# Performance work log

Hardware: AMD Instinct MI355X
Metric: run time of the kernel (lower is better)

Reference implementation:

```python
import jax, jax.numpy as jnp
import numpy as np

EMA_OLD = 0.01  # original: m[z] = m[z]*0.01 + y*0.99
EMA_NEW = 0.99

def setup_inputs() -> dict:
    key = jax.random.key(0)
    k1, k2, k3, k4 = jax.random.split(key, 4)
    B, n, C, L = 4096, 1024, 64, 64
    y = jax.random.normal(k1, (B, C, L), dtype=jnp.float32)   # encoder latents
    m = jax.random.normal(k2, (n, C, L), dtype=jnp.float32)   # codebook means
    sd = jax.random.uniform(k3, (n, C, L), dtype=jnp.float32) # codebook variances (init ones in orig)
    p = jax.random.uniform(k4, (n,), dtype=jnp.float32)       # cluster counts
    return {"y": y, "m": m, "sd": sd, "p": p}

def reference(y, m, sd, p):
    B, C, L = y.shape
    n = m.shape[0]
    # pairwise squared distances via ||y||^2 - 2 y.m + ||m||^2 (GEMM form)
    yf = y.reshape(B, C * L)
    mf = m.reshape(n, C * L)
    d2 = ((yf * yf).sum(-1, keepdims=True)
          - 2.0 * (yf @ mf.T)
          + (mf * mf).sum(-1)[None, :])            # [B, n]
    z = jnp.argmin(d2, axis=1)                      # [B] assignments
    new_m = m.at[z].set(m[z] * EMA_OLD + y * EMA_NEW)
    # original updates sd using the ALREADY-updated m gathered at z
    mg = new_m[z]
    new_sd = sd.at[z].set((mg - y) ** 2 * EMA_OLD + sd[z] * EMA_NEW)
    return jnp.concatenate([new_m, new_sd], axis=0)  # [2n, C, L]
```

## Files before the change

### kernel.cpp

```cpp
#include <hip/hip_runtime.h>

#define B_ROWS 4096
#define N_CLUST 1024
#define KDIM 4096
#define NKT 32
#define NSTEP 16

#define EMA_OLD 0.01f
#define EMA_NEW 0.99f
#define MARGIN 2.0f
#define PSCALE 16.0f

typedef unsigned short ushortT;
typedef _Float16 half8 __attribute__((ext_vector_type(8)));
typedef float f32x16 __attribute__((ext_vector_type(16)));

#define WS_WINNER_OFF 0
#define WS_Z_OFF      4096
#define WS_YY_OFF     20480
#define WS_MM_OFF     36864
#define WS_P_OFF      65536
#define WS_YHI_OFF    (WS_P_OFF + 33554432)
#define WS_MHI_OFF    (WS_YHI_OFF + 33554432)
#define WS_END        (WS_MHI_OFF + 8388608)

__global__ __launch_bounds__(256) void convert_sumsq(
    const float* __restrict__ ysrc, const float* __restrict__ msrc,
    ushortT* __restrict__ yhi, ushortT* __restrict__ mhi,
    float* __restrict__ yy, float* __restrict__ mm) {
    const int blk = blockIdx.x;
    const float* src;
    ushortT* hi;
    float* out;
    int row;
    if (blk < B_ROWS) {
        src = ysrc; hi = yhi; out = yy + blk; row = blk;
    } else {
        row = blk - B_ROWS;
        src = msrc; hi = mhi; out = mm + row;
    }
    const int r = row & 63, rb = row >> 6;
    const int t = threadIdx.x;
    float s = 0.f;
#pragma unroll
    for (int h = 0; h < 2; ++h) {
        int ci = h * 256 + t;
        int kt = ci >> 4, p = ci & 15;
        int c = p ^ (r & 15);
        const float* sp = src + ((size_t)row << 12) + kt * 128 + c * 8;
        float4 v0 = *(const float4*)sp;
        float4 v1 = *(const float4*)(sp + 4);
        float vv[8] = {v0.x, v0.y, v0.z, v0.w, v1.x, v1.y, v1.z, v1.w};
        half8 hv;
#pragma unroll
        for (int i = 0; i < 8; ++i) {
            hv[i] = (_Float16)vv[i];
            s += vv[i] * vv[i];
        }
        size_t off = (((size_t)rb * NKT + kt) * 64 + r) * 128 + p * 8;
        *(half8*)(hi + off) = hv;
    }
    for (int off = 32; off > 0; off >>= 1) s += __shfl_down(s, off, 64);
    __shared__ float red[4];
    if ((t & 63) == 0) red[t >> 6] = s;
    __syncthreads();
    if (t == 0) out[0] = red[0] + red[1] + red[2] + red[3];
}

__device__ __forceinline__ void gload_lds16(const void* g, void* l) {
    __builtin_amdgcn_global_load_lds(
        (const __attribute__((address_space(1))) unsigned int*)g,
        (__attribute__((address_space(3))) unsigned int*)l, 16, 0, 0);
}

__device__ __forceinline__ half8 ldfrag_pair(const ushortT* s, int r, int c) {
    int q = r >> 1;
    int sl = ((((r & 1) << 3) | c) ^ (q & 15));
    return *(const half8*)(s + q * 128 + sl * 8);
}

__global__ __launch_bounds__(256, 4) void screen_gemm(
    const ushortT* __restrict__ Ah, const ushortT* __restrict__ Bh,
    short* __restrict__ pws) {
    __shared__ __align__(16) ushortT sA[128 * 64];
    __shared__ __align__(16) ushortT sB[128 * 64];

    const int t = threadIdx.x, w = t >> 6, l = t & 63;
    const int by = blockIdx.x & 7;
    const int kh = (blockIdx.x >> 3) & 3;
    const int bx = blockIdx.x >> 5;
    const int row0 = bx * 128, col0 = by * 128;
    const int wr = (w >> 1) * 64, wc = (w & 1) * 64;
    const int m0 = l & 31, hsel = l >> 5;

    int laneoff[4];
#pragma unroll
    for (int j = 0; j < 4; ++j) {
        int g = w * 4 + j;
        int q = g * 4 + (l >> 4);
        int u = (l & 15) ^ (q & 15);
        int rr = 2 * q + (u >> 3);
        int R = rr & 63;
        int hi3 = (R >> 3) & 1;
        laneoff[j] = R * 256 + ((((hi3 << 3) | ((u & 7) ^ (R & 7)))) << 4);
    }

    f32x16 acc[2][2];
#pragma unroll
    for (int i = 0; i < 2; ++i)
#pragma unroll
        for (int j = 0; j < 2; ++j)
#pragma unroll
            for (int r = 0; r < 16; ++r) acc[i][j][r] = 0.f;

    const int ra0 = wr + m0, ra1 = wr + 32 + m0;
    const int rb0 = wc + m0, rb1 = wc + 32 + m0;

#pragma unroll 2
    for (int i = 0; i < NSTEP; ++i) {
        const int kt_ = kh * (NKT / 4) + (i >> 1);
        const int ks_ = i & 1;
        __syncthreads();
#pragma unroll
        for (int j = 0; j < 4; ++j) {
            const int g = w * 4 + j;
            const int lo = laneoff[j] ^ (ks_ << 7);
            const size_t tbA = ((size_t)((2 * bx + (g >> 3)) * NKT + kt_) << 14);
            const size_t tbB = ((size_t)((2 * by + (g >> 3)) * NKT + kt_) << 14);
            gload_lds16((const char*)Ah + tbA + lo, (char*)sA + g * 1024);
            gload_lds16((const char*)Bh + tbB + lo, (char*)sB + g * 1024);
        }
        __syncthreads();

#pragma unroll
        for (int kk = 0; kk < 4; ++kk) {
            int c = kk * 2 + hsel;
            half8 a0 = ldfrag_pair(sA, ra0, c);
            half8 a1 = ldfrag_pair(sA, ra1, c);
            half8 b0 = ldfrag_pair(sB, rb0, c);
            half8 b1 = ldfrag_pair(sB, rb1, c);
            acc[0][0] = __builtin_amdgcn_mfma_f32_32x32x16_f16(a0, b0, acc[0][0], 0, 0, 0);
            acc[0][1] = __builtin_amdgcn_mfma_f32_32x32x16_f16(a0, b1, acc[0][1], 0, 0, 0);
            acc[1][0] = __builtin_amdgcn_mfma_f32_32x32x16_f16(a1, b0, acc[1][0], 0, 0, 0);
            acc[1][1] = __builtin_amdgcn_mfma_f32_32x32x16_f16(a1, b1, acc[1][1], 0, 0, 0);
        }
    }

    short* pk = pws + (size_t)kh * (B_ROWS * (size_t)N_CLUST);
#pragma unroll
    for (int i = 0; i < 2; ++i)
#pragma unroll
        for (int j = 0; j < 2; ++j) {
            const int gcol = col0 + wc + j * 32 + m0;
#pragma unroll
            for (int r = 0; r < 16; ++r) {
                int ri = (r & 3) + 8 * (r >> 2) + 4 * hsel;
                int grow = row0 + wr + i * 32 + ri;
                float q = fmaxf(fminf(acc[i][j][r] * (-2.0f * PSCALE),
                                      32767.f), -32767.f);
                pk[(size_t)grow * N_CLUST + gcol] = (short)__float2int_rn(q);
            }
        }
}

__global__ __launch_bounds__(256) void rescreen(
    const short* __restrict__ pws, const float* __restrict__ ysrc,
    const float* __restrict__ msrc, const float* __restrict__ yy,
    const float* __restrict__ mm, int* __restrict__ winner) {
    const int row = blockIdx.x * 4 + (threadIdx.x >> 6);
    const int l = threadIdx.x & 63;
    const size_t rb = (size_t)row * N_CLUST;
    const float yyr = yy[row];

    float v[16];
#pragma unroll
    for (int k = 0; k < 16; ++k) {
        int col = l + 64 * k;
        int s = (int)pws[rb + col];
        s += (int)pws[rb + col + (B_ROWS * (size_t)N_CLUST)];
        s += (int)pws[rb + col + 2 * (B_ROWS * (size_t)N_CLUST)];
        s += (int)pws[rb + col + 3 * (B_ROWS * (size_t)N_CLUST)];
        v[k] = yyr + mm[col] + (float)s * (1.0f / PSCALE);
    }

    float mn = v[0];
#pragma unroll
    for (int k = 1; k < 16; ++k) mn = fminf(mn, v[k]);
#pragma unroll
    for (int s = 1; s <= 32; s <<= 1) mn = fminf(mn, __shfl_xor(mn, s, 64));
    const float thr = mn + MARGIN;

    int cnt = 0;
#pragma unroll
    for (int k = 0; k < 16; ++k) cnt += (v[k] <= thr) ? 1 : 0;
#pragma unroll
    for (int s = 1; s <= 32; s <<= 1) cnt += __shfl_xor(cnt, s, 64);

    int zj;
    if (cnt == 1) {
        int cj = 0x7FFFFFFF;
#pragma unroll
        for (int k = 0; k < 16; ++k)
            if (v[k] <= thr) cj = min(cj, l + 64 * k);
#pragma unroll
        for (int s = 1; s <= 32; s <<= 1) cj = min(cj, __shfl_xor(cj, s, 64));
        zj = cj;
    } else {
        double bestd = 1e300;
        int bestj = -1;
        const float4* yp = (const float4*)(ysrc + (size_t)row * KDIM);
        for (int k = 0; k < 16; ++k) {
            unsigned long long mask = __ballot(v[k] <= thr);
            while (mask) {
                int lb = __ffsll((unsigned long long)mask) - 1;
                mask &= mask - 1;
                int j = 64 * k + lb;
                const float4* mp = (const float4*)(msrc + (size_t)j * KDIM);
                double acc = 0.0;
#pragma unroll
                for (int tt = 0; tt < 16; ++tt) {
                    float4 a = yp[l + 64 * tt];
                    float4 b = mp[l + 64 * tt];
                    acc += (double)a.x * b.x + (double)a.y * b.y +
                           (double)a.z * b.z + (double)a.w * b.w;
                }
#pragma unroll
                for (int s = 1; s <= 32; s <<= 1)
                    acc += __shfl_xor(acc, s, 64);
                double d2x = (double)yy[row] - 2.0 * acc + (double)mm[j];
                if (d2x < bestd) { bestd = d2x; bestj = j; }
            }
        }
        zj = bestj;
    }
    if (l == 0) atomicMax(&winner[zj], row);
}

__global__ __launch_bounds__(256) void write_out(
    const float* __restrict__ y, const float* __restrict__ m,
    const float* __restrict__ sd, const int* __restrict__ winner,
    float* __restrict__ out) {
    const int idx = blockIdx.x;
    const int t = threadIdx.x;
    const int w = winner[idx];
    const float4* mp = (const float4*)(m + (size_t)idx * KDIM);
    const float4* sp = (const float4*)(sd + (size_t)idx * KDIM);
    float4* om = (float4*)(out + (size_t)idx * KDIM);
    float4* os = (float4*)(out + (size_t)(N_CLUST + idx) * KDIM);
    if (w >= 0) {
        const float4* yp = (const float4*)(y + (size_t)w * KDIM);
        for (int i = t; i < KDIM / 4; i += 256) {
            float4 mv = mp[i], yv = yp[i], sv = sp[i];
            float4 nm, ns;
            nm.x = mv.x * EMA_OLD + yv.x * EMA_NEW;
            nm.y = mv.y * EMA_OLD + yv.y * EMA_NEW;
            nm.z = mv.z * EMA_OLD + yv.z * EMA_NEW;
            nm.w = mv.w * EMA_OLD + yv.w * EMA_NEW;
            float dx = nm.x - yv.x, dy = nm.y - yv.y;
            float dz = nm.z - yv.z, dw = nm.w - yv.w;
            ns.x = dx * dx * EMA_OLD + sv.x * EMA_NEW;
            ns.y = dy * dy * EMA_OLD + sv.y * EMA_NEW;
            ns.z = dz * dz * EMA_OLD + sv.z * EMA_NEW;
            ns.w = dw * dw * EMA_OLD + sv.w * EMA_NEW;
            om[i] = nm;
            os[i] = ns;
        }
    } else {
        for (int i = t; i < KDIM / 4; i += 256) {
            om[i] = mp[i];
            os[i] = sp[i];
        }
    }
}

extern "C" void kernel_launch(void* const* d_in, const int* in_sizes, int n_in,
                              void* d_out, int out_size, void* d_ws,
                              size_t ws_size, hipStream_t stream) {
    const float* y  = (const float*)d_in[0];
    const float* m  = (const float*)d_in[1];
    const float* sd = (const float*)d_in[2];
    float* out = (float*)d_out;

    char* ws = (char*)d_ws;
    int* winner = (int*)(ws + WS_WINNER_OFF);
    float* yy   = (float*)(ws + WS_YY_OFF);
    float* mm   = (float*)(ws + WS_MM_OFF);
    short* pws  = (short*)(ws + WS_P_OFF);
    ushortT* yhi = (ushortT*)(ws + WS_YHI_OFF);
    ushortT* mhi = (ushortT*)(ws + WS_MHI_OFF);

    hipMemsetAsync(winner, 0xFF, 4096, stream);

    convert_sumsq<<<B_ROWS + N_CLUST, 256, 0, stream>>>(y, m, yhi, mhi, yy, mm);

    screen_gemm<<<(B_ROWS / 128) * (N_CLUST / 128) * 4, 256, 0, stream>>>(
        yhi, mhi, pws);

    rescreen<<<B_ROWS / 4, 256, 0, stream>>>(pws, y, m, yy, mm, winner);

    write_out<<<N_CLUST, 256, 0, stream>>>(y, m, sd, winner, out);
}
```

Before: 217.7 us.

## Vectorize partial-sum reads in rescreen, use top-2 check, fold winner init

```diff
diff --git a/kernel.cpp b/kernel.cpp
--- a/kernel.cpp
+++ b/kernel.cpp
@@ -10,13 +10,14 @@
 #define EMA_NEW 0.99f
 #define MARGIN 2.0f
 #define PSCALE 16.0f
+#define PLANE ((size_t)B_ROWS * N_CLUST)
 
 typedef unsigned short ushortT;
 typedef _Float16 half8 __attribute__((ext_vector_type(8)));
+typedef short short8v __attribute__((ext_vector_type(8)));
 typedef float f32x16 __attribute__((ext_vector_type(16)));
 
 #define WS_WINNER_OFF 0
-#define WS_Z_OFF      4096
 #define WS_YY_OFF     20480
 #define WS_MM_OFF     36864
 #define WS_P_OFF      65536
@@ -27,7 +28,8 @@
 __global__ __launch_bounds__(256) void convert_sumsq(
     const float* __restrict__ ysrc, const float* __restrict__ msrc,
     ushortT* __restrict__ yhi, ushortT* __restrict__ mhi,
-    float* __restrict__ yy, float* __restrict__ mm) {
+    float* __restrict__ yy, float* __restrict__ mm,
+    int* __restrict__ winner) {
     const int blk = blockIdx.x;
     const float* src;
     ushortT* hi;
@@ -38,6 +40,7 @@
     } else {
         row = blk - B_ROWS;
         src = msrc; hi = mhi; out = mm + row;
+        if (threadIdx.x == 0) winner[row] = -1;
     }
     const int r = row & 63, rb = row >> 6;
     const int t = threadIdx.x;
@@ -146,7 +149,7 @@
         }
     }
 
-    short* pk = pws + (size_t)kh * (B_ROWS * (size_t)N_CLUST);
+    short* pk = pws + (size_t)kh * PLANE;
 #pragma unroll
     for (int i = 0; i < 2; ++i)
 #pragma unroll
@@ -170,51 +173,67 @@
     const int row = blockIdx.x * 4 + (threadIdx.x >> 6);
     const int l = threadIdx.x & 63;
     const size_t rb = (size_t)row * N_CLUST;
-    const float yyr = yy[row];
-
+
+    int sacc[16];
+#pragma unroll
+    for (int q = 0; q < 16; ++q) sacc[q] = 0;
+    const short* base = pws + rb + l * 16;
+#pragma unroll
+    for (int pl = 0; pl < 4; ++pl) {
+        const short8v* sp = (const short8v*)(base + pl * PLANE);
+        short8v x0 = sp[0], x1 = sp[1];
+#pragma unroll
+        for (int e = 0; e < 8; ++e) {
+            sacc[e] += (int)x0[e];
+            sacc[8 + e] += (int)x1[e];
+        }
+    }
     float v[16];
-#pragma unroll
-    for (int k = 0; k < 16; ++k) {
-        int col = l + 64 * k;
-        int s = (int)pws[rb + col];
-        s += (int)pws[rb + col + (B_ROWS * (size_t)N_CLUST)];
-        s += (int)pws[rb + col + 2 * (B_ROWS * (size_t)N_CLUST)];
-        s += (int)pws[rb + col + 3 * (B_ROWS * (size_t)N_CLUST)];
-        v[k] = yyr + mm[col] + (float)s * (1.0f / PSCALE);
-    }
-
-    float mn = v[0];
-#pragma unroll
-    for (int k = 1; k < 16; ++k) mn = fminf(mn, v[k]);
-#pragma unroll
-    for (int s = 1; s <= 32; s <<= 1) mn = fminf(mn, __shfl_xor(mn, s, 64));
-    const float thr = mn + MARGIN;
-
-    int cnt = 0;
-#pragma unroll
-    for (int k = 0; k < 16; ++k) cnt += (v[k] <= thr) ? 1 : 0;
-#pragma unroll
-    for (int s = 1; s <= 32; s <<= 1) cnt += __shfl_xor(cnt, s, 64);
+    const float4* mmv = (const float4*)(mm + l * 16);
+#pragma unroll
+    for (int h = 0; h < 4; ++h) {
+        float4 mv = mmv[h];
+        v[h * 4 + 0] = mv.x + (float)sacc[h * 4 + 0] * (1.0f / PSCALE);
+        v[h * 4 + 1] = mv.y + (float)sacc[h * 4 + 1] * (1.0f / PSCALE);
+        v[h * 4 + 2] = mv.z + (float)sacc[h * 4 + 2] * (1.0f / PSCALE);
+        v[h * 4 + 3] = mv.w + (float)sacc[h * 4 + 3] * (1.0f / PSCALE);
+    }
+
+    float m1 = v[0], m2 = 3.0e38f;
+    int a1 = l * 16;
+#pragma unroll
+    for (int q = 1; q < 16; ++q) {
+        float x = v[q];
+        if (x < m1) { m2 = m1; m1 = x; a1 = l * 16 + q; }
+        else m2 = fminf(m2, x);
+    }
+#pragma unroll
+    for (int s = 1; s <= 32; s <<= 1) {
+        float o1 = __shfl_xor(m1, s, 64);
+        int ob = __shfl_xor(a1, s, 64);
+        float o2 = __shfl_xor(m2, s, 64);
+        if (o1 < m1 || (o1 == m1 && ob < a1)) {
+            m2 = fminf(o2, m1); m1 = o1; a1 = ob;
+        } else {
+            m2 = fminf(m2, o1);
+        }
+    }
 
     int zj;
-    if (cnt == 1) {
-        int cj = 0x7FFFFFFF;
-#pragma unroll
-        for (int k = 0; k < 16; ++k)
-            if (v[k] <= thr) cj = min(cj, l + 64 * k);
-#pragma unroll
-        for (int s = 1; s <= 32; s <<= 1) cj = min(cj, __shfl_xor(cj, s, 64));
-        zj = cj;
+    if (m2 - m1 > MARGIN) {
+        zj = a1;
     } else {
+        const float thr = m1 + MARGIN;
         double bestd = 1e300;
-        int bestj = -1;
+        int bestj = 0x7FFFFFFF;
+        const float yyr = yy[row];
         const float4* yp = (const float4*)(ysrc + (size_t)row * KDIM);
-        for (int k = 0; k < 16; ++k) {
-            unsigned long long mask = __ballot(v[k] <= thr);
+        for (int q = 0; q < 16; ++q) {
+            unsigned long long mask = __ballot(v[q] <= thr);
             while (mask) {
                 int lb = __ffsll((unsigned long long)mask) - 1;
                 mask &= mask - 1;
-                int j = 64 * k + lb;
+                int j = lb * 16 + q;
                 const float4* mp = (const float4*)(msrc + (size_t)j * KDIM);
                 double acc = 0.0;
 #pragma unroll
@@ -227,8 +246,10 @@
 #pragma unroll
                 for (int s = 1; s <= 32; s <<= 1)
                     acc += __shfl_xor(acc, s, 64);
-                double d2x = (double)yy[row] - 2.0 * acc + (double)mm[j];
-                if (d2x < bestd) { bestd = d2x; bestj = j; }
+                double d2x = (double)yyr - 2.0 * acc + (double)mm[j];
+                if (d2x < bestd || (d2x == bestd && j < bestj)) {
+                    bestd = d2x; bestj = j;
+                }
             }
         }
         zj = bestj;
@@ -289,9 +310,8 @@
     ushortT* yhi = (ushortT*)(ws + WS_YHI_OFF);
     ushortT* mhi = (ushortT*)(ws + WS_MHI_OFF);
 
-    hipMemsetAsync(winner, 0xFF, 4096, stream);
-
-    convert_sumsq<<<B_ROWS + N_CLUST, 256, 0, stream>>>(y, m, yhi, mhi, yy, mm);
+    convert_sumsq<<<B_ROWS + N_CLUST, 256, 0, stream>>>(
+        y, m, yhi, mhi, yy, mm, winner);
 
     screen_gemm<<<(B_ROWS / 128) * (N_CLUST / 128) * 4, 256, 0, stream>>>(
         yhi, mhi, pws);
```

After: 215.4 us. About the same (-1.0%).
